# Kernel optimization log

Measured on AMD Instinct MI355X. Metric: run time of the kernel, lower is better.

The kernel has to match this reference:

```python
import jax, jax.numpy as jnp
import numpy as np

B, LQ, LK, NF = 8, 8192, 1024, 64


def setup_inputs() -> dict:
    key = jax.random.key(0)
    k1, k2, k3, k4, k5 = jax.random.split(key, 5)
    x = jax.random.normal(k1, (B, LQ, NF), dtype=jnp.float32)
    kv = jax.random.normal(k2, (B, LK, NF), dtype=jnp.float32)
    # 1x1 submanifold convolutions == per-point linear maps (no bias)
    scale = 1.0 / np.sqrt(NF)
    Wq = jax.random.normal(k3, (NF, NF), dtype=jnp.float32) * scale
    Wk = jax.random.normal(k4, (NF, NF), dtype=jnp.float32) * scale
    Wv = jax.random.normal(k5, (NF, NF), dtype=jnp.float32) * scale
    return {"x": x, "kv": kv, "Wq": Wq, "Wk": Wk, "Wv": Wv}


def reference(x, kv, Wq, Wk, Wv):
    # q/k/v projections (1x1 convs on sparse features = dense matmuls)
    q = jnp.einsum("bqd,de->bqe", x, Wq)    # [B, LQ, NF]
    k = jnp.einsum("bkd,de->bke", kv, Wk)   # [B, LK, NF]
    v = jnp.einsum("bkd,de->bke", kv, Wv)   # [B, LK, NF]
    # per-batch (block-diagonal / ragged) attention: e = q k^T, softmax over keys, @ v
    scores = jnp.einsum("bqe,bke->bqk", q, k)        # [B, LQ, LK] (no scaling, as in source)
    attn = jax.nn.softmax(scores, axis=-1)
    out = jnp.einsum("bqk,bke->bqe", attn, v)        # [B, LQ, NF]
    return out
```

## Files before the change

### kernel.cpp

```cpp
#include <hip/hip_runtime.h>
#include <hip/hip_fp16.h>

constexpr int B_  = 8;
constexpr int LQ  = 8192;
constexpr int LK  = 1024;
constexpr int NF  = 64;

typedef _Float16 f16x8  __attribute__((ext_vector_type(8)));
typedef float    f32x16 __attribute__((ext_vector_type(16)));

#define MFMA32(a, b, c) __builtin_amdgcn_mfma_f32_32x32x16_f16((a), (b), (c), 0, 0, 0)

__device__ __forceinline__ f16x8 ldf(const _Float16* p) { return *(const f16x8*)p; }

__device__ __forceinline__ f16x8 ldfrag_f32(const float* row, int t, int h) {
  int off = 32 * (t >> 1) + 16 * (t & 1) + 4 * h;
  float4 r0 = *(const float4*)(row + off);
  float4 r1 = *(const float4*)(row + off + 8);
  f16x8 r;
  r[0] = (_Float16)r0.x; r[1] = (_Float16)r0.y; r[2] = (_Float16)r0.z; r[3] = (_Float16)r0.w;
  r[4] = (_Float16)r1.x; r[5] = (_Float16)r1.y; r[6] = (_Float16)r1.z; r[7] = (_Float16)r1.w;
  return r;
}

__device__ __forceinline__ f16x8 pk8(const f32x16 c, int u) {
  int b = u * 8;
  auto p0 = __builtin_amdgcn_cvt_pkrtz(c[b],     c[b + 1]);
  auto p1 = __builtin_amdgcn_cvt_pkrtz(c[b + 2], c[b + 3]);
  auto p2 = __builtin_amdgcn_cvt_pkrtz(c[b + 4], c[b + 5]);
  auto p3 = __builtin_amdgcn_cvt_pkrtz(c[b + 6], c[b + 7]);
  f16x8 r;
  r[0] = p0[0]; r[1] = p0[1]; r[2] = p1[0]; r[3] = p1[1];
  r[4] = p2[0]; r[5] = p2[1]; r[6] = p3[0]; r[7] = p3[1];
  return r;
}

__device__ __forceinline__ int w_src_idx(int idx) {
  int chunk = idx >> 9, r9 = idx & 511;
  int lane_ = r9 >> 3, j = r9 & 7;
  int m32 = lane_ & 31, h = lane_ >> 5;
  int tt = chunk & 3;
  int din  = 32 * (tt >> 1) + 16 * (tt & 1) + 4 * h + 8 * (j >> 2) + (j & 3);
  int dout = (chunk >> 2) * 32 + m32;
  return din * 64 + dout;
}

__device__ __forceinline__ void dma16(const _Float16* g, _Float16* l) {
  __builtin_amdgcn_global_load_lds(
      (const __attribute__((address_space(1))) unsigned int*)g,
      (__attribute__((address_space(3))) unsigned int*)l, 16, 0, 0);
}

__device__ __forceinline__ void tile_barrier() {
  asm volatile("s_waitcnt vmcnt(0)\n\ts_barrier" ::: "memory");
}

__global__ __launch_bounds__(256) void kv_proj_kernel(
    const float* __restrict__ kv, const float* __restrict__ Wk,
    const float* __restrict__ Wv, _Float16* __restrict__ KV) {
  __shared__ __align__(16) _Float16 wlds[8192];

  const int t    = threadIdx.x;
  const int wave = t >> 6, lane = t & 63, m32 = lane & 31, h = lane >> 5;
  const int bb   = blockIdx.x >> 3;
  const int kblk = blockIdx.x & 7;

#pragma unroll
  for (int i = 0; i < 16; ++i) {
    int idx = t + 256 * i;
    int s = w_src_idx(idx);
    wlds[idx]        = (_Float16)Wk[s];
    wlds[4096 + idx] = (_Float16)Wv[s];
  }

  const int key = kblk * 128 + wave * 32 + m32;
  const float* kvrow = kv + ((size_t)bb * LK + key) * NF;
  f16x8 kvf[4];
#pragma unroll
  for (int tt = 0; tt < 4; ++tt) kvf[tt] = ldfrag_f32(kvrow, tt, h);
  __syncthreads();

  const int T = bb * 16 + kblk * 2 + (wave >> 1);
  _Float16* tile = KV + (size_t)T * 8192;
  const int kb = wave & 1;

#pragma unroll
  for (int mb = 0; mb < 2; ++mb) {
    f32x16 C = {};
#pragma unroll
    for (int tt = 0; tt < 4; ++tt)
      C = MFMA32(ldf(&wlds[(mb * 4 + tt) * 512 + lane * 8]), kvf[tt], C);
#pragma unroll
    for (int u = 0; u < 2; ++u)
      *(f16x8*)(tile + ((size_t)(kb * 4 + 2 * mb + u)) * 512 + lane * 8) = pk8(C, u);
  }
#pragma unroll
  for (int nb = 0; nb < 2; ++nb) {
    f32x16 C = {};
#pragma unroll
    for (int tt = 0; tt < 4; ++tt)
      C = MFMA32(kvf[tt], ldf(&wlds[4096 + (nb * 4 + tt) * 512 + lane * 8]), C);
#pragma unroll
    for (int u = 0; u < 2; ++u)
      *(f16x8*)(tile + 4096 + ((size_t)(nb * 4 + 2 * kb + u)) * 512 + lane * 8) = pk8(C, u);
  }
}

__global__ __launch_bounds__(512, 2) void attn_kernel(
    const float* __restrict__ x, const float* __restrict__ Wq,
    const _Float16* __restrict__ KV, float* __restrict__ out) {
  __shared__ __align__(16) _Float16 lds[2][2][8192];
  __shared__ __align__(16) _Float16 wq_l[4096];

  const int t    = threadIdx.x;
  const int wave = t >> 6, lane = t & 63, m32 = lane & 31, h = lane >> 5;
  const int wq_i = wave & 3, wg = wave >> 2;
  const int b    = blockIdx.x >> 5;
  const int qw_base = (blockIdx.x & 31) * 256 + wq_i * 64;
  constexpr float LOG2E = 1.44269504088896f;

#pragma unroll
  for (int i = 0; i < 8; ++i) {
    int idx = t + 512 * i;
    wq_l[idx] = (_Float16)(Wq[w_src_idx(idx)] * LOG2E);
  }

  const _Float16* Kg = KV + ((size_t)b * 16 + wg * 8) * 8192;
#pragma unroll
  for (int q = 0; q < 4; ++q) {
    int ch = wq_i * 4 + q;
    dma16(Kg + ch * 512 + lane * 8, &lds[wg][0][ch * 512]);
  }
  __syncthreads();

  f16x8 qb[2][4];
  {
    f16x8 wa[2][4];
#pragma unroll
    for (int mb = 0; mb < 2; ++mb)
#pragma unroll
      for (int tt = 0; tt < 4; ++tt)
        wa[mb][tt] = ldf(&wq_l[(mb * 4 + tt) * 512 + lane * 8]);
#pragma unroll
    for (int s = 0; s < 2; ++s) {
      const float* xrow = x + ((size_t)b * LQ + qw_base + s * 32 + m32) * NF;
      f16x8 xf[4];
#pragma unroll
      for (int tt = 0; tt < 4; ++tt) xf[tt] = ldfrag_f32(xrow, tt, h);
#pragma unroll
      for (int mb = 0; mb < 2; ++mb) {
        f32x16 C = {};
#pragma unroll
        for (int tt = 0; tt < 4; ++tt) C = MFMA32(wa[mb][tt], xf[tt], C);
        qb[s][2 * mb]     = pk8(C, 0);
        qb[s][2 * mb + 1] = pk8(C, 1);
      }
    }
  }

  f16x8 ones;
#pragma unroll
  for (int j = 0; j < 8; ++j) ones[j] = (_Float16)1.0f;

  float  m_s[2] = {-1e30f, -1e30f};
  f32x16 lacc[2] = {};
  f32x16 oacc[2][2] = {};

  for (int tile = 0; tile < 8; ++tile) {
    tile_barrier();
    if (tile < 7) {
      const _Float16* nt = Kg + (size_t)(tile + 1) * 8192;
      _Float16* nb_ = &lds[wg][(tile + 1) & 1][0];
#pragma unroll
      for (int q = 0; q < 4; ++q) {
        int ch = wq_i * 4 + q;
        dma16(nt + ch * 512 + lane * 8, nb_ + ch * 512);
      }
    }
    const _Float16* tb = &lds[wg][tile & 1][0];

    f32x16 st[2][2] = {};
#pragma unroll
    for (int kb = 0; kb < 2; ++kb)
#pragma unroll
      for (int tt = 0; tt < 4; ++tt) {
        f16x8 a = ldf(tb + (size_t)(kb * 4 + tt) * 512 + lane * 8);
        st[0][kb] = MFMA32(a, qb[0][tt], st[0][kb]);
        st[1][kb] = MFMA32(a, qb[1][tt], st[1][kb]);
      }

    f16x8 pa[2][4];
#pragma unroll
    for (int s = 0; s < 2; ++s) {
      float tmax = st[s][0][0];
#pragma unroll
      for (int kb = 0; kb < 2; ++kb)
#pragma unroll
        for (int r = 1 - kb; r < 16; ++r) tmax = fmaxf(tmax, st[s][kb][r]);
      tmax = fmaxf(tmax, __shfl_xor(tmax, 32));

      if (__ballot(tmax > m_s[s]) != 0) {
        float mnew  = fmaxf(m_s[s], tmax);
        float alpha = __builtin_amdgcn_exp2f(m_s[s] - mnew);
        m_s[s] = mnew;
        float ar[16];
#pragma unroll
        for (int r = 0; r < 16; ++r)
          ar[r] = __shfl(alpha, (r & 3) + 8 * (r >> 2) + 4 * h);
#pragma unroll
        for (int r = 0; r < 16; ++r) {
          lacc[s][r]    *= ar[r];
          oacc[s][0][r] *= ar[r];
          oacc[s][1][r] *= ar[r];
        }
      }

#pragma unroll
      for (int kb = 0; kb < 2; ++kb)
#pragma unroll
        for (int r = 0; r < 16; ++r)
          st[s][kb][r] = __builtin_amdgcn_exp2f(st[s][kb][r] - m_s[s]);

#pragma unroll
      for (int kb = 0; kb < 2; ++kb) {
        pa[s][2 * kb]     = pk8(st[s][kb], 0);
        pa[s][2 * kb + 1] = pk8(st[s][kb], 1);
      }
#pragma unroll
      for (int tt = 0; tt < 4; ++tt) lacc[s] = MFMA32(pa[s][tt], ones, lacc[s]);
    }

#pragma unroll
    for (int nb = 0; nb < 2; ++nb)
#pragma unroll
      for (int tt = 0; tt < 4; ++tt) {
        f16x8 vb = ldf(tb + 4096 + (size_t)(nb * 4 + tt) * 512 + lane * 8);
        oacc[0][nb] = MFMA32(pa[0][tt], vb, oacc[0][nb]);
        oacc[1][nb] = MFMA32(pa[1][tt], vb, oacc[1][nb]);
      }
  }

  float* mrg_m = (float*)&lds[0][0][0];
  float* mrg_l = mrg_m + 256;
  float* mrg_o = mrg_l + 4096;

#pragma unroll
  for (int s = 0; s < 2; ++s) {
    __syncthreads();
    if (wg == 1) {
      mrg_m[wq_i * 64 + lane] = m_s[s];
#pragma unroll
      for (int r = 0; r < 16; ++r)
        mrg_l[(wq_i * 16 + r) * 64 + lane] = lacc[s][r];
#pragma unroll
      for (int nb = 0; nb < 2; ++nb)
#pragma unroll
        for (int r = 0; r < 16; ++r)
          mrg_o[(wq_i * 32 + nb * 16 + r) * 64 + lane] = oacc[s][nb][r];
    }
    __syncthreads();
    if (wg == 0) {
      float mh = mrg_m[wq_i * 64 + lane];
      float mx = fmaxf(m_s[s], mh);
      float al = __builtin_amdgcn_exp2f(m_s[s] - mx);
      float ah = __builtin_amdgcn_exp2f(mh - mx);
      float alr[16], ahr[16];
#pragma unroll
      for (int r = 0; r < 16; ++r) {
        int src = (r & 3) + 8 * (r >> 2) + 4 * h;
        alr[r] = __shfl(al, src);
        ahr[r] = __shfl(ah, src);
      }
#pragma unroll
      for (int r = 0; r < 16; ++r) {
        float lh = mrg_l[(wq_i * 16 + r) * 64 + lane];
        float linv = 1.0f / (alr[r] * lacc[s][r] + ahr[r] * lh);
        int q_out = qw_base + s * 32 + (r & 3) + 8 * (r >> 2) + 4 * h;
        float* orow = out + ((size_t)b * LQ + q_out) * NF + m32;
        float o0 = alr[r] * oacc[s][0][r] + ahr[r] * mrg_o[(wq_i * 32 + r) * 64 + lane];
        float o1 = alr[r] * oacc[s][1][r] + ahr[r] * mrg_o[(wq_i * 32 + 16 + r) * 64 + lane];
        orow[0]  = o0 * linv;
        orow[32] = o1 * linv;
      }
    }
  }
}

extern "C" void kernel_launch(void* const* d_in, const int* in_sizes, int n_in,
                              void* d_out, int out_size, void* d_ws, size_t ws_size,
                              hipStream_t stream) {
  const float* x  = (const float*)d_in[0];
  const float* kv = (const float*)d_in[1];
  const float* Wq = (const float*)d_in[2];
  const float* Wk = (const float*)d_in[3];
  const float* Wv = (const float*)d_in[4];
  float* out = (float*)d_out;

  _Float16* KV = (_Float16*)d_ws;

  kv_proj_kernel<<<B_ * (LK / 128), 256, 0, stream>>>(kv, Wk, Wv, KV);
  attn_kernel<<<B_ * (LQ / 256), 512, 0, stream>>>(x, Wq, KV, out);
}
```

Measured before the change: 111.9 us.

## Split keys across four wave groups with 32-key tiles and tree merge

The K/V workspace is re-tiled into 32-key tiles, and each 512-thread block now handles 128 queries with four wave groups that each process a quarter of the keys. Partial softmax states are then combined in a two-level LDS tree merge. This doubles the block count and requests higher occupancy via launch bounds, in exchange for more merge work and smaller MFMA batches per tile. It also adds a lazy rescale threshold that skips the rescale unless the running max grows by more than 3 (in log2 units), and unrolls the tile loop by two.

```diff
diff --git a/kernel.cpp b/kernel.cpp
--- a/kernel.cpp
+++ b/kernel.cpp
@@ -55,6 +55,34 @@
   asm volatile("s_waitcnt vmcnt(0)\n\ts_barrier" ::: "memory");
 }
 
+__device__ __forceinline__ void store_state(float* mrg, int base, int lane, float m,
+                                            const f32x16& l, const f32x16& o0, const f32x16& o1) {
+  mrg[base + lane] = m;
+#pragma unroll
+  for (int r = 0; r < 16; ++r) {
+    mrg[base + 64 +        r * 64 + lane] = l[r];
+    mrg[base + 64 + 1024 + r * 64 + lane] = o0[r];
+    mrg[base + 64 + 2048 + r * 64 + lane] = o1[r];
+  }
+}
+
+__device__ __forceinline__ void merge_state(float* mrg, int base, int lane, int h, float& m,
+                                            f32x16& l, f32x16& o0, f32x16& o1) {
+  float mp = mrg[base + lane];
+  float mn = fmaxf(m, mp);
+  float a  = __builtin_amdgcn_exp2f(m  - mn);
+  float bq = __builtin_amdgcn_exp2f(mp - mn);
+  m = mn;
+#pragma unroll
+  for (int r = 0; r < 16; ++r) {
+    int src = (r & 3) + 8 * (r >> 2) + 4 * h;
+    float ar = __shfl(a, src), br = __shfl(bq, src);
+    l[r]  = ar * l[r]  + br * mrg[base + 64 +        r * 64 + lane];
+    o0[r] = ar * o0[r] + br * mrg[base + 64 + 1024 + r * 64 + lane];
+    o1[r] = ar * o1[r] + br * mrg[base + 64 + 2048 + r * 64 + lane];
+  }
+}
+
 __global__ __launch_bounds__(256) void kv_proj_kernel(
     const float* __restrict__ kv, const float* __restrict__ Wk,
     const float* __restrict__ Wv, _Float16* __restrict__ KV) {
@@ -80,9 +108,7 @@
   for (int tt = 0; tt < 4; ++tt) kvf[tt] = ldfrag_f32(kvrow, tt, h);
   __syncthreads();
 
-  const int T = bb * 16 + kblk * 2 + (wave >> 1);
-  _Float16* tile = KV + (size_t)T * 8192;
-  const int kb = wave & 1;
+  _Float16* base = KV + ((size_t)bb * 32 + kblk * 4 + wave) * 4096;
 
 #pragma unroll
   for (int mb = 0; mb < 2; ++mb) {
@@ -92,7 +118,7 @@
       C = MFMA32(ldf(&wlds[(mb * 4 + tt) * 512 + lane * 8]), kvf[tt], C);
 #pragma unroll
     for (int u = 0; u < 2; ++u)
-      *(f16x8*)(tile + ((size_t)(kb * 4 + 2 * mb + u)) * 512 + lane * 8) = pk8(C, u);
+      *(f16x8*)(base + (size_t)(2 * mb + u) * 512 + lane * 8) = pk8(C, u);
   }
 #pragma unroll
   for (int nb = 0; nb < 2; ++nb) {
@@ -102,21 +128,21 @@
       C = MFMA32(kvf[tt], ldf(&wlds[4096 + (nb * 4 + tt) * 512 + lane * 8]), C);
 #pragma unroll
     for (int u = 0; u < 2; ++u)
-      *(f16x8*)(tile + 4096 + ((size_t)(nb * 4 + 2 * kb + u)) * 512 + lane * 8) = pk8(C, u);
-  }
-}
-
-__global__ __launch_bounds__(512, 2) void attn_kernel(
+      *(f16x8*)(base + 2048 + (size_t)(nb * 2 + u) * 512 + lane * 8) = pk8(C, u);
+  }
+}
+
+__global__ __launch_bounds__(512, 4) void attn_kernel(
     const float* __restrict__ x, const float* __restrict__ Wq,
     const _Float16* __restrict__ KV, float* __restrict__ out) {
-  __shared__ __align__(16) _Float16 lds[2][2][8192];
+  __shared__ __align__(16) _Float16 lds[4][2][4096];
   __shared__ __align__(16) _Float16 wq_l[4096];
 
   const int t    = threadIdx.x;
   const int wave = t >> 6, lane = t & 63, m32 = lane & 31, h = lane >> 5;
-  const int wq_i = wave & 3, wg = wave >> 2;
-  const int b    = blockIdx.x >> 5;
-  const int qw_base = (blockIdx.x & 31) * 256 + wq_i * 64;
+  const int wq_i = wave & 1, wg = wave >> 1;
+  const int b    = blockIdx.x >> 6;
+  const int qw_base = (blockIdx.x & 63) * 128 + wq_i * 64;
   constexpr float LOG2E = 1.44269504088896f;
 
 #pragma unroll
@@ -125,7 +151,7 @@
     wq_l[idx] = (_Float16)(Wq[w_src_idx(idx)] * LOG2E);
   }
 
-  const _Float16* Kg = KV + ((size_t)b * 16 + wg * 8) * 8192;
+  const _Float16* Kg = KV + ((size_t)b * 32 + wg * 8) * 4096;
 #pragma unroll
   for (int q = 0; q < 4; ++q) {
     int ch = wq_i * 4 + q;
@@ -166,10 +192,11 @@
   f32x16 lacc[2] = {};
   f32x16 oacc[2][2] = {};
 
+#pragma unroll 2
   for (int tile = 0; tile < 8; ++tile) {
     tile_barrier();
     if (tile < 7) {
-      const _Float16* nt = Kg + (size_t)(tile + 1) * 8192;
+      const _Float16* nt = Kg + (size_t)(tile + 1) * 4096;
       _Float16* nb_ = &lds[wg][(tile + 1) & 1][0];
 #pragma unroll
       for (int q = 0; q < 4; ++q) {
@@ -179,27 +206,23 @@
     }
     const _Float16* tb = &lds[wg][tile & 1][0];
 
-    f32x16 st[2][2] = {};
-#pragma unroll
-    for (int kb = 0; kb < 2; ++kb)
-#pragma unroll
-      for (int tt = 0; tt < 4; ++tt) {
-        f16x8 a = ldf(tb + (size_t)(kb * 4 + tt) * 512 + lane * 8);
-        st[0][kb] = MFMA32(a, qb[0][tt], st[0][kb]);
-        st[1][kb] = MFMA32(a, qb[1][tt], st[1][kb]);
-      }
-
-    f16x8 pa[2][4];
+    f32x16 st[2] = {};
+#pragma unroll
+    for (int tt = 0; tt < 4; ++tt) {
+      f16x8 a = ldf(tb + (size_t)tt * 512 + lane * 8);
+      st[0] = MFMA32(a, qb[0][tt], st[0]);
+      st[1] = MFMA32(a, qb[1][tt], st[1]);
+    }
+
+    f16x8 pa[2][2];
 #pragma unroll
     for (int s = 0; s < 2; ++s) {
-      float tmax = st[s][0][0];
-#pragma unroll
-      for (int kb = 0; kb < 2; ++kb)
-#pragma unroll
-        for (int r = 1 - kb; r < 16; ++r) tmax = fmaxf(tmax, st[s][kb][r]);
+      float tmax = st[s][0];
+#pragma unroll
+      for (int r = 1; r < 16; ++r) tmax = fmaxf(tmax, st[s][r]);
       tmax = fmaxf(tmax, __shfl_xor(tmax, 32));
 
-      if (__ballot(tmax > m_s[s]) != 0) {
+      if (__ballot(tmax > m_s[s] + 3.0f) != 0) {
         float mnew  = fmaxf(m_s[s], tmax);
         float alpha = __builtin_amdgcn_exp2f(m_s[s] - mnew);
         m_s[s] = mnew;
@@ -216,71 +239,49 @@
       }
 
 #pragma unroll
-      for (int kb = 0; kb < 2; ++kb)
-#pragma unroll
-        for (int r = 0; r < 16; ++r)
-          st[s][kb][r] = __builtin_amdgcn_exp2f(st[s][kb][r] - m_s[s]);
-
-#pragma unroll
-      for (int kb = 0; kb < 2; ++kb) {
-        pa[s][2 * kb]     = pk8(st[s][kb], 0);
-        pa[s][2 * kb + 1] = pk8(st[s][kb], 1);
-      }
-#pragma unroll
-      for (int tt = 0; tt < 4; ++tt) lacc[s] = MFMA32(pa[s][tt], ones, lacc[s]);
+      for (int r = 0; r < 16; ++r)
+        st[s][r] = __builtin_amdgcn_exp2f(st[s][r] - m_s[s]);
+
+      pa[s][0] = pk8(st[s], 0);
+      pa[s][1] = pk8(st[s], 1);
+      lacc[s] = MFMA32(pa[s][0], ones, lacc[s]);
+      lacc[s] = MFMA32(pa[s][1], ones, lacc[s]);
     }
 
 #pragma unroll
     for (int nb = 0; nb < 2; ++nb)
 #pragma unroll
-      for (int tt = 0; tt < 4; ++tt) {
-        f16x8 vb = ldf(tb + 4096 + (size_t)(nb * 4 + tt) * 512 + lane * 8);
-        oacc[0][nb] = MFMA32(pa[0][tt], vb, oacc[0][nb]);
-        oacc[1][nb] = MFMA32(pa[1][tt], vb, oacc[1][nb]);
-      }
-  }
-
-  float* mrg_m = (float*)&lds[0][0][0];
-  float* mrg_l = mrg_m + 256;
-  float* mrg_o = mrg_l + 4096;
-
+      for (int u = 0; u < 2; ++u) {
+        f16x8 vb = ldf(tb + 2048 + (size_t)(nb * 2 + u) * 512 + lane * 8);
+        oacc[0][nb] = MFMA32(pa[0][u], vb, oacc[0][nb]);
+        oacc[1][nb] = MFMA32(pa[1][u], vb, oacc[1][nb]);
+      }
+  }
+
+  float* mrg = (float*)&lds[0][0][0];
 #pragma unroll
   for (int s = 0; s < 2; ++s) {
     __syncthreads();
-    if (wg == 1) {
-      mrg_m[wq_i * 64 + lane] = m_s[s];
-#pragma unroll
-      for (int r = 0; r < 16; ++r)
-        mrg_l[(wq_i * 16 + r) * 64 + lane] = lacc[s][r];
-#pragma unroll
-      for (int nb = 0; nb < 2; ++nb)
-#pragma unroll
-        for (int r = 0; r < 16; ++r)
-          mrg_o[(wq_i * 32 + nb * 16 + r) * 64 + lane] = oacc[s][nb][r];
-    }
+    int slot = ((wg >> 1) * 2 + wq_i) * 3136;
+    if (wg & 1) store_state(mrg, slot, lane, m_s[s], lacc[s], oacc[s][0], oacc[s][1]);
+    __syncthreads();
+    if (!(wg & 1)) merge_state(mrg, slot, lane, h, m_s[s], lacc[s], oacc[s][0], oacc[s][1]);
+  }
+#pragma unroll
+  for (int s = 0; s < 2; ++s) {
+    __syncthreads();
+    int slot = wq_i * 3136;
+    if (wg == 2) store_state(mrg, slot, lane, m_s[s], lacc[s], oacc[s][0], oacc[s][1]);
     __syncthreads();
     if (wg == 0) {
-      float mh = mrg_m[wq_i * 64 + lane];
-      float mx = fmaxf(m_s[s], mh);
-      float al = __builtin_amdgcn_exp2f(m_s[s] - mx);
-      float ah = __builtin_amdgcn_exp2f(mh - mx);
-      float alr[16], ahr[16];
+      merge_state(mrg, slot, lane, h, m_s[s], lacc[s], oacc[s][0], oacc[s][1]);
 #pragma unroll
       for (int r = 0; r < 16; ++r) {
-        int src = (r & 3) + 8 * (r >> 2) + 4 * h;
-        alr[r] = __shfl(al, src);
-        ahr[r] = __shfl(ah, src);
-      }
-#pragma unroll
-      for (int r = 0; r < 16; ++r) {
-        float lh = mrg_l[(wq_i * 16 + r) * 64 + lane];
-        float linv = 1.0f / (alr[r] * lacc[s][r] + ahr[r] * lh);
+        float linv = 1.0f / lacc[s][r];
         int q_out = qw_base + s * 32 + (r & 3) + 8 * (r >> 2) + 4 * h;
         float* orow = out + ((size_t)b * LQ + q_out) * NF + m32;
-        float o0 = alr[r] * oacc[s][0][r] + ahr[r] * mrg_o[(wq_i * 32 + r) * 64 + lane];
-        float o1 = alr[r] * oacc[s][1][r] + ahr[r] * mrg_o[(wq_i * 32 + 16 + r) * 64 + lane];
-        orow[0]  = o0 * linv;
-        orow[32] = o1 * linv;
+        orow[0]  = oacc[s][0][r] * linv;
+        orow[32] = oacc[s][1][r] * linv;
       }
     }
   }
@@ -299,5 +300,5 @@
   _Float16* KV = (_Float16*)d_ws;
 
   kv_proj_kernel<<<B_ * (LK / 128), 256, 0, stream>>>(kv, Wk, Wv, KV);
-  attn_kernel<<<B_ * (LQ / 256), 512, 0, stream>>>(x, Wq, KV, out);
-}
+  attn_kernel<<<B_ * (LQ / 128), 512, 0, stream>>>(x, Wq, KV, out);
+}
```

Measured after the change: 363.1 us. 224% more time.
